# Performance work log

Measured on AMD Instinct MI355X. Metric: run time of the kernel, lower is better.

## Reference

```python
import jax, jax.numpy as jnp
import numpy as np

THRESH = 0.2  # contact probability threshold from _make_graph default


def setup_inputs() -> dict:
    key = jax.random.key(0)
    ks = jax.random.split(key, 10)
    L, D, K, M = 1024, 640, 32, 64
    S = jax.random.normal(ks[0], (L, D), jnp.float32)
    P = jax.random.uniform(ks[1], (L, L), jnp.float32)
    P = 0.5 * (P + P.T)  # symmetric base-pair probability matrix
    xyz = jax.random.normal(ks[2], (L, 3), jnp.float32) * 10.0  # Angstrom-scale C1' coords
    rbf_mu = jnp.linspace(0.0, 30.0, K).astype(jnp.float32)     # RBF centers over 0-30 A
    rbf_sigma = jax.random.uniform(ks[3], (K,), jnp.float32, 0.5, 2.0)
    W_edge = jax.random.normal(ks[4], (K + 2, M), jnp.float32) * 0.05
    b_edge = jnp.zeros((M,), jnp.float32)
    W_node = jax.random.normal(ks[5], (D, M), jnp.float32) * 0.05
    w_out = jax.random.normal(ks[6], (M,), jnp.float32) * 0.1
    return {"S": S, "P": P, "xyz": xyz, "rbf_mu": rbf_mu, "rbf_sigma": rbf_sigma,
            "W_edge": W_edge, "b_edge": b_edge, "W_node": W_node, "w_out": w_out}


def reference(S, P, xyz, rbf_mu, rbf_sigma, W_edge, b_edge, W_node, w_out):
    """Graph construction (_make_graph) + one SE3-style gated coordinate update.

    Edges: backbone (j == i+1, etype=0, pij=1) and high-prob contacts
    (P[i,j] > THRESH, j > i+2, etype=1, pij=P[i,j]). Edge scalars are
    [etype, pij, rbf(d)] exactly as in _make_graph; edge vectors are
    xyz[j]-xyz[i]. Computed in dense masked form for jit-compatibility.
    """
    L = xyz.shape[0]
    rel = xyz[None, :, :] - xyz[:, None, :]                      # (L,L,3) xyz[j]-xyz[i]
    # safe norm: eps avoids nan grad on zero diagonal (diagonal is masked out anyway)
    d = jnp.sqrt(jnp.sum(rel * rel, axis=-1, keepdims=True) + 1e-12)  # (L,L,1)
    rbf_feat = jnp.exp(-(d - rbf_mu) ** 2 / (2.0 * rbf_sigma ** 2))   # (L,L,K)

    idx = jnp.arange(L)
    backbone = idx[None, :] == idx[:, None] + 1                  # j == i+1
    contact = (P > THRESH) & (idx[None, :] > idx[:, None] + 2)   # skip j <= i+2
    mask = backbone | contact                                    # (L,L)

    etype = contact.astype(S.dtype)                              # 0 backbone, 1 contact
    pij = jnp.where(backbone, jnp.asarray(1.0, S.dtype), P)
    e_scalar = jnp.concatenate([etype[..., None], pij[..., None], rbf_feat], axis=-1)  # (L,L,K+2)

    # gather-compute: message from edge scalars + destination-node scalars
    node_proj = S @ W_node                                       # (L,M)
    msg = jax.nn.relu(jnp.einsum('ijk,km->ijm', e_scalar, W_edge) + b_edge
                      + node_proj[None, :, :])                   # (L,L,M)
    gate = jax.nn.sigmoid(msg @ w_out) * mask.astype(S.dtype)    # (L,L)

    # scatter: equivariant coordinate update, sum of gated edge vectors per node
    xyz_out = xyz + jnp.einsum('ij,ijc->ic', gate, rel)          # (L,3)
    return xyz_out
```

## Files before the change

kernel.cpp:

```cpp
#include <hip/hip_runtime.h>
#include <math.h>

#define LL 1024
#define DD 640
#define KK 32
#define MM 64
#define THRESH 0.2f
#define LOG2E 1.4426950408889634f

#define NPROJ_OFF  0
#define NPROJC_OFF (NPROJ_OFF + LL * MM)
#define WRT_OFF    (NPROJC_OFF + LL * MM)
#define W1_OFF     (WRT_OFF + 1024)
#define EA_OFF     (W1_OFF + MM)
#define EB_OFF     (EA_OFF + KK)
#define EC_OFF     (EB_OFF + KK)
#define XYZ4_OFF   (EC_OFF + KK)

typedef float f32x4_t __attribute__((ext_vector_type(4)));
typedef short bf16x8_t __attribute__((ext_vector_type(8)));

union FragU { unsigned int u[4]; bf16x8_t v; };

#if __has_builtin(__builtin_amdgcn_sqrtf)
#define FSQRT __builtin_amdgcn_sqrtf
#else
#define FSQRT sqrtf
#endif

#if __has_builtin(__builtin_amdgcn_exp2f)
#define EXP2F __builtin_amdgcn_exp2f
#else
#define EXP2F(x) __expf((x) * 0.6931471805599453f)
#endif

__device__ __forceinline__ unsigned int pack_bf(float hi, float lo) {
    return __builtin_amdgcn_perm(__float_as_uint(hi), __float_as_uint(lo), 0x07060302u);
}

__global__ __launch_bounds__(256) void prep_sk(
    const float* __restrict__ S, const float* __restrict__ xyz,
    const float* __restrict__ rbf_mu, const float* __restrict__ rbf_sigma,
    const float* __restrict__ W_edge, const float* __restrict__ b_edge,
    const float* __restrict__ W_node, float* __restrict__ ws)
{
    const int b = blockIdx.x;
    const int t = threadIdx.x;
    if (b < 256) {
        __shared__ float red[4][64][4];
        const int lane = t & 63;
        const int wave = t >> 6;
        const int r0   = (b >> 2) * 16;
        const int n0   = (b & 3) * 16;
        const int col  = lane & 15;
        const int quad = lane >> 4;

        f32x4_t acc = {0.f, 0.f, 0.f, 0.f};
        const float* arow = S + (size_t)(r0 + col) * DD + wave * 160 + quad * 8;
        const float* bcol = W_node + (size_t)(wave * 160 + quad * 8) * MM + n0 + col;

        #pragma unroll
        for (int ks = 0; ks < 5; ++ks) {
            const float4 a0 = *(const float4*)(arow + ks * 32);
            const float4 a1 = *(const float4*)(arow + ks * 32 + 4);
            FragU A;
            A.u[0] = pack_bf(a0.y, a0.x); A.u[1] = pack_bf(a0.w, a0.z);
            A.u[2] = pack_bf(a1.y, a1.x); A.u[3] = pack_bf(a1.w, a1.z);
            const float* bk = bcol + (size_t)ks * 32 * MM;
            const float b0 = bk[0 * MM], b1 = bk[1 * MM], b2 = bk[2 * MM], b3 = bk[3 * MM];
            const float b4 = bk[4 * MM], b5 = bk[5 * MM], b6 = bk[6 * MM], b7 = bk[7 * MM];
            FragU B;
            B.u[0] = pack_bf(b1, b0); B.u[1] = pack_bf(b3, b2);
            B.u[2] = pack_bf(b5, b4); B.u[3] = pack_bf(b7, b6);
            acc = __builtin_amdgcn_mfma_f32_16x16x32_bf16(A.v, B.v, acc, 0, 0, 0);
        }
        red[wave][lane][0] = acc[0];
        red[wave][lane][1] = acc[1];
        red[wave][lane][2] = acc[2];
        red[wave][lane][3] = acc[3];
        __syncthreads();
        const int lr  = t & 63;
        const int reg = t >> 6;
        const float v = (red[0][lr][reg] + red[1][lr][reg])
                      + (red[2][lr][reg] + red[3][lr][reg]);
        const int row = r0 + (lr >> 4) * 4 + reg;
        const int cc  = n0 + (lr & 15);
        const float vb = v + b_edge[cc];
        ws[NPROJ_OFF  + (size_t)row * MM + cc] = vb;
        ws[NPROJC_OFF + (size_t)row * MM + cc] = vb + W_edge[cc];
    } else {
        unsigned short* wrt = (unsigned short*)(ws + WRT_OFF);
        if (t < MM) ws[W1_OFF + t] = W_edge[MM + t];
        if (t < KK) {
            const float s  = rbf_sigma[t];
            const float m_ = rbf_mu[t];
            const float inv = 1.0f / (2.0f * s * s);
            ws[EA_OFF + t] = -LOG2E * inv;
            ws[EB_OFF + t] =  2.0f * LOG2E * inv * m_;
            ws[EC_OFF + t] = -LOG2E * inv * m_ * m_;
        }
        for (int idx = t; idx < KK * MM; idx += 256) {
            const int m = idx >> 5, k = idx & 31;
            unsigned int u = __float_as_uint(W_edge[(2 + k) * MM + m]);
            u = (u + 0x7fffu + ((u >> 16) & 1u)) >> 16;
            wrt[idx] = (unsigned short)u;
        }
        for (int n = t; n < LL; n += 256) {
            float4 v;
            v.x = xyz[3 * n + 0]; v.y = xyz[3 * n + 1];
            v.z = xyz[3 * n + 2]; v.w = 0.0f;
            *(float4*)(ws + XYZ4_OFF + 4 * n) = v;
        }
    }
}

__global__ __launch_bounds__(256) void edge_kernel6(
    const float* __restrict__ P, const float* __restrict__ w_out,
    const float* __restrict__ ws, float* __restrict__ out)
{
    const int tid  = threadIdx.x;
    const int lane = tid & 63;
    const int wave = tid >> 6;
    const int quad = lane >> 4;
    const int col  = lane & 15;
    __shared__ float4 lxyz[LL];
    __shared__ float sred[4][3];

    const float* __restrict__ nproj  = ws + NPROJ_OFF;
    const float* __restrict__ nprojc = ws + NPROJC_OFF;
    const float4* __restrict__ xyz4  = (const float4*)(ws + XYZ4_OFF);
    const unsigned short* __restrict__ wrt = (const unsigned short*)(ws + WRT_OFF);

    #pragma unroll
    for (int n = tid; n < LL; n += 256) lxyz[n] = xyz4[n];

    FragU ar[4];
    float w1r[16], wvr[16];
    float aj[8], bj[8], cj[8];
    #pragma unroll
    for (int mt = 0; mt < 4; ++mt) {
        const uint4 w = *(const uint4*)(wrt + (mt * 16 + col) * KK + quad * 8);
        ar[mt].u[0] = w.x; ar[mt].u[1] = w.y; ar[mt].u[2] = w.z; ar[mt].u[3] = w.w;
        const f32x4_t w1 = *(const f32x4_t*)(ws + W1_OFF + mt * 16 + quad * 4);
        const f32x4_t wo = *(const f32x4_t*)(w_out + mt * 16 + quad * 4);
        #pragma unroll
        for (int r = 0; r < 4; ++r) { w1r[mt * 4 + r] = w1[r]; wvr[mt * 4 + r] = wo[r]; }
    }
    #pragma unroll
    for (int j = 0; j < 8; ++j) {
        aj[j] = ws[EA_OFF + quad * 8 + j];
        bj[j] = ws[EB_OFF + quad * 8 + j];
        cj[j] = ws[EC_OFF + quad * 8 + j];
    }
    __syncthreads();

    const int i = (int)blockIdx.x;
    const float4 xo = lxyz[i];
    const float xi0 = xo.x, xi1 = xo.y, xi2 = xo.z;
    const int len = (LL - 1) - i;
    float ax = 0.f, ay = 0.f, az = 0.f;
    const float* __restrict__ prow = P + (size_t)i * LL;

    for (int base = wave * 64; base < len; base += 256) {
        const int jo = base + lane;
        const bool valid = jo < len;
        const int jc_o = valid ? (i + 1 + jo) : (LL - 1);
        const float p_own = prow[jc_o];
        const float4 xj = lxyz[jc_o];
        const float rx = xj.x - xi0, ry = xj.y - xi1, rz = xj.z - xi2;
        const bool msk = valid && ((jo == 0) || ((jo >= 2) && (p_own > THRESH)));

        float res[4];
        #pragma unroll
        for (int ct = 0; ct < 4; ++ct) {
            const int jo_n = base + ct * 16 + col;
            int jc = i + 1 + jo_n;
            jc = (jc < LL) ? jc : (LL - 1);
            const float p_n = prow[jc];
            const float4 xn = lxyz[jc];
            const float dx = xn.x - xi0, dy = xn.y - xi1, dz = xn.z - xi2;
            const float q2 = fmaf(dx, dx, fmaf(dy, dy, fmaf(dz, dz, 1e-12f)));
            const float d_n = FSQRT(q2);
            const bool bb = (jo_n == 0);
            const float peff = bb ? 1.0f : p_n;
            const float* npr = (bb ? nproj : nprojc) + (size_t)jc * MM;

            float e[8];
            #pragma unroll
            for (int j = 0; j < 8; ++j)
                e[j] = EXP2F(fmaf(aj[j], q2, fmaf(bj[j], d_n, cj[j])));
            FragU bf;
            bf.u[0] = pack_bf(e[1], e[0]); bf.u[1] = pack_bf(e[3], e[2]);
            bf.u[2] = pack_bf(e[5], e[4]); bf.u[3] = pack_bf(e[7], e[6]);

            float g = 0.0f;
            #pragma unroll
            for (int mt = 0; mt < 4; ++mt) {
                f32x4_t c0 = *(const f32x4_t*)(npr + mt * 16 + quad * 4);
                c0[0] = fmaf(peff, w1r[mt*4+0], c0[0]);
                c0[1] = fmaf(peff, w1r[mt*4+1], c0[1]);
                c0[2] = fmaf(peff, w1r[mt*4+2], c0[2]);
                c0[3] = fmaf(peff, w1r[mt*4+3], c0[3]);
                c0 = __builtin_amdgcn_mfma_f32_16x16x32_bf16(ar[mt].v, bf.v, c0, 0, 0, 0);
                g = fmaf(fmaxf(c0[0], 0.f), wvr[mt*4+0], g);
                g = fmaf(fmaxf(c0[1], 0.f), wvr[mt*4+1], g);
                g = fmaf(fmaxf(c0[2], 0.f), wvr[mt*4+2], g);
                g = fmaf(fmaxf(c0[3], 0.f), wvr[mt*4+3], g);
            }
            g += __shfl_xor(g, 16, 64);
            g += __shfl_xor(g, 32, 64);
            res[ct] = g;
        }
        float gd = res[0];
        gd = (quad == 1) ? res[1] : gd;
        gd = (quad == 2) ? res[2] : gd;
        gd = (quad == 3) ? res[3] : gd;
        const float gate = msk ? (1.0f / (1.0f + __expf(-gd))) : 0.0f;
        ax = fmaf(gate, rx, ax);
        ay = fmaf(gate, ry, ay);
        az = fmaf(gate, rz, az);
    }

    #pragma unroll
    for (int off = 32; off > 0; off >>= 1) {
        ax += __shfl_down(ax, off, 64);
        ay += __shfl_down(ay, off, 64);
        az += __shfl_down(az, off, 64);
    }
    if (lane == 0) { sred[wave][0] = ax; sred[wave][1] = ay; sred[wave][2] = az; }
    __syncthreads();
    if (tid == 0) {
        const float tx = (sred[0][0] + sred[1][0]) + (sred[2][0] + sred[3][0]);
        const float ty = (sred[0][1] + sred[1][1]) + (sred[2][1] + sred[3][1]);
        const float tz = (sred[0][2] + sred[1][2]) + (sred[2][2] + sred[3][2]);
        out[i * 3 + 0] = xi0 + tx;
        out[i * 3 + 1] = xi1 + ty;
        out[i * 3 + 2] = xi2 + tz;
    }
}

extern "C" void kernel_launch(void* const* d_in, const int* in_sizes, int n_in,
                              void* d_out, int out_size, void* d_ws, size_t ws_size,
                              hipStream_t stream) {
    const float* S         = (const float*)d_in[0];
    const float* P         = (const float*)d_in[1];
    const float* xyz       = (const float*)d_in[2];
    const float* rbf_mu    = (const float*)d_in[3];
    const float* rbf_sigma = (const float*)d_in[4];
    const float* W_edge    = (const float*)d_in[5];
    const float* b_edge    = (const float*)d_in[6];
    const float* W_node    = (const float*)d_in[7];
    const float* w_out     = (const float*)d_in[8];
    float* out = (float*)d_out;
    float* ws  = (float*)d_ws;

    prep_sk<<<257, 256, 0, stream>>>(S, xyz, rbf_mu, rbf_sigma,
                                     W_edge, b_edge, W_node, ws);
    edge_kernel6<<<LL, 256, 0, stream>>>(P, w_out, ws, out);
}
```

Before: 100.8 us.

## Parallelize edge kernel over destination columns with atomic scatter to outputs

Restructures the edge kernel so each block owns a destination node j and loops over sources i<j-2. The destination's node projection then stays in registers instead of being reloaded per edge, and P is read along a row thanks to its symmetry. Backbone edges are handled separately by one wave in scalar code. Per-source contributions are accumulated in shared memory and scattered to the output with atomics, and prep now initializes out with xyz. This removes the per-edge nproj gather but adds up to ~3L atomics per block and makes the summation order nondeterministic.

```diff
diff --git a/kernel.cpp b/kernel.cpp
--- a/kernel.cpp
+++ b/kernel.cpp
@@ -42,7 +42,8 @@
     const float* __restrict__ S, const float* __restrict__ xyz,
     const float* __restrict__ rbf_mu, const float* __restrict__ rbf_sigma,
     const float* __restrict__ W_edge, const float* __restrict__ b_edge,
-    const float* __restrict__ W_node, float* __restrict__ ws)
+    const float* __restrict__ W_node, float* __restrict__ ws,
+    float* __restrict__ out)
 {
     const int b = blockIdx.x;
     const int t = threadIdx.x;
@@ -111,31 +112,34 @@
             v.z = xyz[3 * n + 2]; v.w = 0.0f;
             *(float4*)(ws + XYZ4_OFF + 4 * n) = v;
         }
-    }
-}
-
-__global__ __launch_bounds__(256) void edge_kernel6(
+        for (int idx = t; idx < 3 * LL; idx += 256) out[idx] = xyz[idx];
+    }
+}
+
+__global__ __launch_bounds__(256) void edge_colpar(
     const float* __restrict__ P, const float* __restrict__ w_out,
     const float* __restrict__ ws, float* __restrict__ out)
 {
+    __shared__ float4 lacc[LL];
     const int tid  = threadIdx.x;
     const int lane = tid & 63;
     const int wave = tid >> 6;
     const int quad = lane >> 4;
     const int col  = lane & 15;
-    __shared__ float4 lxyz[LL];
-    __shared__ float sred[4][3];
-
-    const float* __restrict__ nproj  = ws + NPROJ_OFF;
-    const float* __restrict__ nprojc = ws + NPROJC_OFF;
-    const float4* __restrict__ xyz4  = (const float4*)(ws + XYZ4_OFF);
+
+    const float4* __restrict__ xyz4 = (const float4*)(ws + XYZ4_OFF);
     const unsigned short* __restrict__ wrt = (const unsigned short*)(ws + WRT_OFF);
 
-    #pragma unroll
-    for (int n = tid; n < LL; n += 256) lxyz[n] = xyz4[n];
+    const int j   = (LL - 1) - (int)blockIdx.x;
+    const int len = j - 2;
+
+    {
+        const float4 z = {0.f, 0.f, 0.f, 0.f};
+        for (int n = tid; n < j; n += 256) lacc[n] = z;
+    }
 
     FragU ar[4];
-    float w1r[16], wvr[16];
+    float w1r[16], wvr[16], cjr[16];
     float aj[8], bj[8], cj[8];
     #pragma unroll
     for (int mt = 0; mt < 4; ++mt) {
@@ -143,52 +147,72 @@
         ar[mt].u[0] = w.x; ar[mt].u[1] = w.y; ar[mt].u[2] = w.z; ar[mt].u[3] = w.w;
         const f32x4_t w1 = *(const f32x4_t*)(ws + W1_OFF + mt * 16 + quad * 4);
         const f32x4_t wo = *(const f32x4_t*)(w_out + mt * 16 + quad * 4);
-        #pragma unroll
-        for (int r = 0; r < 4; ++r) { w1r[mt * 4 + r] = w1[r]; wvr[mt * 4 + r] = wo[r]; }
+        const f32x4_t cc = *(const f32x4_t*)(ws + NPROJC_OFF + (size_t)j * MM + mt * 16 + quad * 4);
+        #pragma unroll
+        for (int r = 0; r < 4; ++r) {
+            w1r[mt * 4 + r] = w1[r];
+            wvr[mt * 4 + r] = wo[r];
+            cjr[mt * 4 + r] = cc[r];
+        }
     }
     #pragma unroll
-    for (int j = 0; j < 8; ++j) {
-        aj[j] = ws[EA_OFF + quad * 8 + j];
-        bj[j] = ws[EB_OFF + quad * 8 + j];
-        cj[j] = ws[EC_OFF + quad * 8 + j];
-    }
+    for (int jj = 0; jj < 8; ++jj) {
+        aj[jj] = ws[EA_OFF + quad * 8 + jj];
+        bj[jj] = ws[EB_OFF + quad * 8 + jj];
+        cj[jj] = ws[EC_OFF + quad * 8 + jj];
+    }
+
+    const float4 xo = xyz4[j];
+    const float xi0 = xo.x, xi1 = xo.y, xi2 = xo.z;
+    const float* __restrict__ prow = P + (size_t)j * LL;
+
     __syncthreads();
 
-    const int i = (int)blockIdx.x;
-    const float4 xo = lxyz[i];
-    const float xi0 = xo.x, xi1 = xo.y, xi2 = xo.z;
-    const int len = (LL - 1) - i;
-    float ax = 0.f, ay = 0.f, az = 0.f;
-    const float* __restrict__ prow = P + (size_t)i * LL;
+    if (wave == 0 && j >= 1) {
+        const int m = lane;
+        const float4 xb = xyz4[j - 1];
+        const float bx = xi0 - xb.x, by = xi1 - xb.y, bz = xi2 - xb.z;
+        const float q2b = fmaf(bx, bx, fmaf(by, by, fmaf(bz, bz, 1e-12f)));
+        const float db = FSQRT(q2b);
+        float acc = ws[NPROJ_OFF + (size_t)j * MM + m] + ws[W1_OFF + m];
+        const uint4 wa = *(const uint4*)(wrt + m * KK);
+        const uint4 wb = *(const uint4*)(wrt + m * KK + 8);
+        const unsigned int wu[8] = {wa.x, wa.y, wa.z, wa.w, wb.x, wb.y, wb.z, wb.w};
+        #pragma unroll
+        for (int k = 0; k < KK; ++k) {
+            const float r = EXP2F(fmaf(ws[EA_OFF + k], q2b,
+                              fmaf(ws[EB_OFF + k], db, ws[EC_OFF + k])));
+            const unsigned int h = (k & 1) ? (wu[k >> 1] & 0xffff0000u)
+                                           : (wu[k >> 1] << 16);
+            acc = fmaf(r, __uint_as_float(h), acc);
+        }
+        float gg = fmaxf(acc, 0.f) * w_out[m];
+        #pragma unroll
+        for (int off = 32; off > 0; off >>= 1) gg += __shfl_down(gg, off, 64);
+        if (lane == 0) {
+            const float gate = 1.0f / (1.0f + __expf(-gg));
+            float4 v;
+            v.x = gate * bx; v.y = gate * by; v.z = gate * bz; v.w = 0.f;
+            lacc[j - 1] = v;
+        }
+    }
 
     for (int base = wave * 64; base < len; base += 256) {
-        const int jo = base + lane;
-        const bool valid = jo < len;
-        const int jc_o = valid ? (i + 1 + jo) : (LL - 1);
-        const float p_own = prow[jc_o];
-        const float4 xj = lxyz[jc_o];
-        const float rx = xj.x - xi0, ry = xj.y - xi1, rz = xj.z - xi2;
-        const bool msk = valid && ((jo == 0) || ((jo >= 2) && (p_own > THRESH)));
-
         float res[4];
         #pragma unroll
         for (int ct = 0; ct < 4; ++ct) {
-            const int jo_n = base + ct * 16 + col;
-            int jc = i + 1 + jo_n;
-            jc = (jc < LL) ? jc : (LL - 1);
-            const float p_n = prow[jc];
-            const float4 xn = lxyz[jc];
-            const float dx = xn.x - xi0, dy = xn.y - xi1, dz = xn.z - xi2;
+            int ic = base + ct * 16 + col;
+            ic = (ic < len) ? ic : (len - 1);
+            const float p_n = prow[ic];
+            const float4 xn = xyz4[ic];
+            const float dx = xi0 - xn.x, dy = xi1 - xn.y, dz = xi2 - xn.z;
             const float q2 = fmaf(dx, dx, fmaf(dy, dy, fmaf(dz, dz, 1e-12f)));
-            const float d_n = FSQRT(q2);
-            const bool bb = (jo_n == 0);
-            const float peff = bb ? 1.0f : p_n;
-            const float* npr = (bb ? nproj : nprojc) + (size_t)jc * MM;
+            const float dn = FSQRT(q2);
 
             float e[8];
             #pragma unroll
-            for (int j = 0; j < 8; ++j)
-                e[j] = EXP2F(fmaf(aj[j], q2, fmaf(bj[j], d_n, cj[j])));
+            for (int jj = 0; jj < 8; ++jj)
+                e[jj] = EXP2F(fmaf(aj[jj], q2, fmaf(bj[jj], dn, cj[jj])));
             FragU bf;
             bf.u[0] = pack_bf(e[1], e[0]); bf.u[1] = pack_bf(e[3], e[2]);
             bf.u[2] = pack_bf(e[5], e[4]); bf.u[3] = pack_bf(e[7], e[6]);
@@ -196,11 +220,11 @@
             float g = 0.0f;
             #pragma unroll
             for (int mt = 0; mt < 4; ++mt) {
-                f32x4_t c0 = *(const f32x4_t*)(npr + mt * 16 + quad * 4);
-                c0[0] = fmaf(peff, w1r[mt*4+0], c0[0]);
-                c0[1] = fmaf(peff, w1r[mt*4+1], c0[1]);
-                c0[2] = fmaf(peff, w1r[mt*4+2], c0[2]);
-                c0[3] = fmaf(peff, w1r[mt*4+3], c0[3]);
+                f32x4_t c0;
+                c0[0] = fmaf(p_n, w1r[mt*4+0], cjr[mt*4+0]);
+                c0[1] = fmaf(p_n, w1r[mt*4+1], cjr[mt*4+1]);
+                c0[2] = fmaf(p_n, w1r[mt*4+2], cjr[mt*4+2]);
+                c0[3] = fmaf(p_n, w1r[mt*4+3], cjr[mt*4+3]);
                 c0 = __builtin_amdgcn_mfma_f32_16x16x32_bf16(ar[mt].v, bf.v, c0, 0, 0, 0);
                 g = fmaf(fmaxf(c0[0], 0.f), wvr[mt*4+0], g);
                 g = fmaf(fmaxf(c0[1], 0.f), wvr[mt*4+1], g);
@@ -211,31 +235,30 @@
             g += __shfl_xor(g, 32, 64);
             res[ct] = g;
         }
-        float gd = res[0];
-        gd = (quad == 1) ? res[1] : gd;
-        gd = (quad == 2) ? res[2] : gd;
-        gd = (quad == 3) ? res[3] : gd;
-        const float gate = msk ? (1.0f / (1.0f + __expf(-gd))) : 0.0f;
-        ax = fmaf(gate, rx, ax);
-        ay = fmaf(gate, ry, ay);
-        az = fmaf(gate, rz, az);
-    }
-
-    #pragma unroll
-    for (int off = 32; off > 0; off >>= 1) {
-        ax += __shfl_down(ax, off, 64);
-        ay += __shfl_down(ay, off, 64);
-        az += __shfl_down(az, off, 64);
-    }
-    if (lane == 0) { sred[wave][0] = ax; sred[wave][1] = ay; sred[wave][2] = az; }
+
+        const int i_own = base + lane;
+        if (i_own < len) {
+            float gd = res[0];
+            gd = (quad == 1) ? res[1] : gd;
+            gd = (quad == 2) ? res[2] : gd;
+            gd = (quad == 3) ? res[3] : gd;
+            const float p_own = prow[i_own];
+            const float4 xn = xyz4[i_own];
+            const float gate = (p_own > THRESH) ? (1.0f / (1.0f + __expf(-gd))) : 0.0f;
+            float4 v = lacc[i_own];
+            v.x = fmaf(gate, xi0 - xn.x, v.x);
+            v.y = fmaf(gate, xi1 - xn.y, v.y);
+            v.z = fmaf(gate, xi2 - xn.z, v.z);
+            lacc[i_own] = v;
+        }
+    }
+
     __syncthreads();
-    if (tid == 0) {
-        const float tx = (sred[0][0] + sred[1][0]) + (sred[2][0] + sred[3][0]);
-        const float ty = (sred[0][1] + sred[1][1]) + (sred[2][1] + sred[3][1]);
-        const float tz = (sred[0][2] + sred[1][2]) + (sred[2][2] + sred[3][2]);
-        out[i * 3 + 0] = xi0 + tx;
-        out[i * 3 + 1] = xi1 + ty;
-        out[i * 3 + 2] = xi2 + tz;
+    for (int n = tid; n < j; n += 256) {
+        const float4 v = lacc[n];
+        atomicAdd(out + n * 3 + 0, v.x);
+        atomicAdd(out + n * 3 + 1, v.y);
+        atomicAdd(out + n * 3 + 2, v.z);
     }
 }
 
@@ -255,6 +278,6 @@
     float* ws  = (float*)d_ws;
 
     prep_sk<<<257, 256, 0, stream>>>(S, xyz, rbf_mu, rbf_sigma,
-                                     W_edge, b_edge, W_node, ws);
-    edge_kernel6<<<LL, 256, 0, stream>>>(P, w_out, ws, out);
-}
+                                     W_edge, b_edge, W_node, ws, out);
+    edge_colpar<<<LL, 256, 0, stream>>>(P, w_out, ws, out);
+}
```

New measurement: 159.4 us. 1.58x slower.
